# Performance work log

Measured on AMD Instinct MI355X. Metric: run time of the kernel, lower is better.

## Reference

```python
import jax, jax.numpy as jnp
import numpy as np

TEMPERATURE = 0.07
THRESHOLD = 0.7
NUM = 21          # config['data_loader']['args']['class_num']
EPS = 1e-12       # F.normalize eps
NEG_BIG = 1e30


def _nearest_down(x, H, W):
    # torch F.interpolate(mode='nearest'): in_idx = floor(out_idx * in/out)
    Hin, Win = x.shape[-2], x.shape[-1]
    ih = (jnp.arange(H) * Hin) // H
    iw = (jnp.arange(W) * Win) // W
    return x[..., ih[:, None], iw[None, :]]


def _l2n(x):
    return x / jnp.maximum(jnp.linalg.norm(x, axis=1, keepdims=True), EPS)


def setup_inputs() -> dict:
    key = jax.random.key(0)
    ks = jax.random.split(key, 6)
    B, C, H, W = 8, 256, 128, 128
    return {
        "labels": jax.random.randint(ks[0], (B, 512, 512), 0, NUM, dtype=jnp.int64)
        if jax.config.jax_enable_x64 else jax.random.randint(ks[0], (B, 512, 512), 0, NUM, dtype=jnp.int32),
        "features_old": jax.random.normal(ks[1], (B, C, H, W), dtype=jnp.float32),
        "features": jax.random.normal(ks[2], (B, C, H, W), dtype=jnp.float32),
        "outputs_old": jax.random.normal(ks[3], (B, 16, 512, 512), dtype=jnp.float32),
        "outputs": jax.random.normal(ks[4], (B, NUM, 512, 512), dtype=jnp.float32),
        "prototypes": jax.random.normal(ks[5], (NUM, C), dtype=jnp.float32),
        "num_class": 21,
        "num_old_class": 16,
        "num_new_class": 5,
        "epoch": 1,
        "train_step": 1,
        "len_epoch": 100,
    }


def reference(labels, features_old, features, outputs_old, outputs, prototypes,
              num_class, num_old_class, num_new_class, epoch, train_step, len_epoch):
    B, C, H, W = features.shape
    f32 = features.dtype

    # pseudo-label construction
    labels_down = _nearest_down(labels, H, W)                      # [B,H,W] int
    bgr_mask = (labels_down == 0).astype(labels_down.dtype)
    oo = jnp.where(outputs_old < THRESHOLD, 0.0, outputs_old)
    old_pred = jnp.argmax(oo, axis=1)                              # [B,512,512]
    old_down = _nearest_down(old_pred, H, W).astype(labels_down.dtype)
    pseudo = old_down * bgr_mask + labels_down                     # [B,H,W]
    lab = pseudo.reshape(-1)                                       # [N]
    mask = (lab >= 0) & (lab < NUM)

    # [N, C] normalized pixel features
    fa = _l2n(features.transpose(0, 2, 3, 1).reshape(-1, C))
    fo = _l2n(features_old.transpose(0, 2, 3, 1).reshape(-1, C))

    # per-class mean (segment reduce) replacing the python loop over unique labels
    seg = jnp.where(mask, lab, NUM)
    w = mask.astype(f32)
    counts = jax.ops.segment_sum(w, seg, num_segments=NUM + 1)[:NUM]          # [K]
    sum_a = jax.ops.segment_sum(fa * w[:, None], seg, num_segments=NUM + 1)[:NUM]
    sum_o = jax.ops.segment_sum(fo * w[:, None], seg, num_segments=NUM + 1)[:NUM]
    present = counts > 0
    denom = jnp.where(present, counts, 1.0)[:, None]
    anc = jnp.where(present[:, None], sum_a / denom, 0.0)          # [K,C] anchor prototypes
    con_prev = jnp.where(present[:, None], sum_o / denom, 0.0)     # [K,C] old prototypes
    contrast = jax.lax.stop_gradient(jnp.concatenate([anc, con_prev], axis=0))  # [2K,C]

    K = NUM
    eye = jnp.eye(K, dtype=f32)
    rowp = present.astype(f32)                                     # [K]
    colp = jnp.concatenate([rowp, rowp])                           # [2K]
    # labels are unique per row, so R = [I | I]; pos = [0 | I]; neg = 1 - R
    pos_mask = jnp.concatenate([jnp.zeros((K, K), f32), eye], axis=1) * rowp[:, None] * colp[None, :]
    neg_mask = (1.0 - jnp.concatenate([eye, eye], axis=1)) * rowp[:, None] * colp[None, :]

    adc = (anc @ contrast.T) / TEMPERATURE                         # [K,2K]
    # NOTE: faithful to source, negatives use UNshifted logits
    neg = jnp.sum(jnp.exp(adc) * neg_mask, axis=1, keepdims=True)  # [K,1]
    logits_max = jnp.max(jnp.where(colp[None, :] > 0, adc, -NEG_BIG), axis=1, keepdims=True)
    shifted = adc - jax.lax.stop_gradient(logits_max)
    pos_contrast = shifted * pos_mask - jnp.log(jnp.exp(shifted) + neg) * pos_mask

    num = pos_mask.sum(axis=1)
    valid = num > 0
    row_loss = -pos_contrast.sum(axis=1) / jnp.where(valid, num, 1.0)
    loss = jnp.sum(jnp.where(valid, row_loss, 0.0)) / jnp.maximum(jnp.sum(valid.astype(f32)), 1.0)
    return loss
```

## Files before the change

kernel.cpp:

```cpp
#include <hip/hip_runtime.h>
#include <math.h>

#define NPIX   131072
#define CCH    256
#define HW     16384
#define BSTR   4194304
#define NUMC   21
#define KC     5376
#define NREP   16

typedef __attribute__((ext_vector_type(8))) short bf16x8;
typedef __attribute__((ext_vector_type(4))) float f32x4;

static __device__ __forceinline__ uint f2bf(float x) {
    uint u = __builtin_bit_cast(uint, x);
    return (u + 0x7FFFu + ((u >> 16) & 1u)) >> 16;
}
static __device__ __forceinline__ uint ohv(int lbl, int cls, uint iv) {
    return (lbl == cls) ? iv : 0u;
}
static __device__ __forceinline__ float rsq_fast(float x) {
#if __has_builtin(__builtin_amdgcn_rsqf)
    return __builtin_amdgcn_rsqf(x);
#else
    return rsqrtf(x);
#endif
}
static __device__ __forceinline__ uint bfpack_trunc(float x, float y) {
    return __builtin_amdgcn_perm(__builtin_bit_cast(uint, y),
                                 __builtin_bit_cast(uint, x), 0x07060302u);
}

__global__ __launch_bounds__(256) void k_labels(const int* __restrict__ labels,
                                                const float* __restrict__ outputs_old,
                                                int* __restrict__ lab,
                                                float* __restrict__ gcnt)
{
    __shared__ float cnt[NUMC];
    if (threadIdx.x < NUMC) cnt[threadIdx.x] = 0.f;
    __syncthreads();

    int p = blockIdx.x * 256 + threadIdx.x;
    int b = p >> 14;
    int rem = p & 16383;
    int h = rem >> 7;
    int w = rem & 127;
    int ld = labels[b * 262144 + (h * 4) * 512 + (w * 4)];
    int out = ld;
    if (ld == 0) {
        const float* oo = outputs_old + (size_t)b * BSTR + (size_t)(h * 4) * 512 + (w * 4);
        float v0 = oo[0];
        float best = (v0 < 0.7f) ? 0.0f : v0;
        int bi = 0;
        #pragma unroll
        for (int c = 1; c < 16; ++c) {
            float v = oo[(size_t)c * 262144];
            v = (v < 0.7f) ? 0.0f : v;
            if (v > best) { best = v; bi = c; }
        }
        out = bi;
    }
    lab[p] = out;
    unsafeAtomicAdd(&cnt[out], 1.0f);
    __syncthreads();
    if (threadIdx.x < NUMC) unsafeAtomicAdd(&gcnt[threadIdx.x], cnt[threadIdx.x]);
}

__global__ __launch_bounds__(256, 2) void k_msum(const float* __restrict__ fa,
                                                 const float* __restrict__ fo,
                                                 const int* __restrict__ lab,
                                                 float* __restrict__ partA,
                                                 float* __restrict__ partO)
{
    __shared__ ushort tileB[CCH * 128];
    __shared__ float  ssqP[4][128];
    __shared__ float  invnS[128];
    __shared__ int    labS[256];

    const int t = threadIdx.x;
    const int w = t >> 6, l = t & 63;
    const int isO = blockIdx.x & 1;
    const float* __restrict__ src = isO ? fo : fa;
    float* part = isO ? partO : partA;

    const int pbase = (blockIdx.x >> 1) * 256;
    const int img   = pbase >> 14;
    const int hw0   = pbase & 16383;
    const float* g  = src + (size_t)img * BSTR + hw0;

    labS[t] = lab[pbase + t];

    f32x4 acc[2][4];
    #pragma unroll
    for (int m = 0; m < 2; ++m)
        #pragma unroll
        for (int n = 0; n < 4; ++n)
            acc[m][n] = (f32x4){0.f, 0.f, 0.f, 0.f};

#define LOADB(B, i0) do { \
    _Pragma("unroll") \
    for (int i_ = 0; i_ < 8; ++i_) \
        B[i_] = *(const float4*)(gc + (size_t)(w * 64 + 2 * ((i0) + i_) + (l >> 5)) * HW \
                                 + (l & 31) * 4); \
    } while (0)

#define PROCB(B, i0) do { \
    _Pragma("unroll") \
    for (int i_ = 0; i_ < 8; ++i_) { \
        float4 v_ = B[i_]; \
        s4.x += v_.x * v_.x;  s4.y += v_.y * v_.y; \
        s4.z += v_.z * v_.z;  s4.w += v_.w * v_.w; \
        int ch_ = w * 64 + 2 * ((i0) + i_) + (l >> 5); \
        uint lo_ = bfpack_trunc(v_.x, v_.y); \
        uint hi_ = bfpack_trunc(v_.z, v_.w); \
        *(uint2*)((char*)tileB + ch_ * 256 + ((((l & 31) * 8)) ^ ((ch_ & 7) << 4))) = \
            make_uint2(lo_, hi_); \
    } \
    } while (0)

#define KSTEP(c2, ks) do { \
    float4 ivA_ = *(const float4*)&invnS[(ks) * 32 + (l >> 4) * 8]; \
    float4 ivB_ = *(const float4*)&invnS[(ks) * 32 + (l >> 4) * 8 + 4]; \
    uint iv0 = f2bf(ivA_.x), iv1 = f2bf(ivA_.y), iv2 = f2bf(ivA_.z), iv3 = f2bf(ivA_.w); \
    uint iv4 = f2bf(ivB_.x), iv5 = f2bf(ivB_.y), iv6 = f2bf(ivB_.z), iv7 = f2bf(ivB_.w); \
    int4 la_ = *(const int4*)&labS[(c2) * 128 + (ks) * 32 + (l >> 4) * 8]; \
    int4 lb_ = *(const int4*)&labS[(c2) * 128 + (ks) * 32 + (l >> 4) * 8 + 4]; \
    const int cls0_ = l & 15, cls1_ = 16 + (l & 15); \
    uint4 u0_, u1_; \
    u0_.x = ohv(la_.x, cls0_, iv0) | (ohv(la_.y, cls0_, iv1) << 16); \
    u0_.y = ohv(la_.z, cls0_, iv2) | (ohv(la_.w, cls0_, iv3) << 16); \
    u0_.z = ohv(lb_.x, cls0_, iv4) | (ohv(lb_.y, cls0_, iv5) << 16); \
    u0_.w = ohv(lb_.z, cls0_, iv6) | (ohv(lb_.w, cls0_, iv7) << 16); \
    u1_.x = ohv(la_.x, cls1_, iv0) | (ohv(la_.y, cls1_, iv1) << 16); \
    u1_.y = ohv(la_.z, cls1_, iv2) | (ohv(la_.w, cls1_, iv3) << 16); \
    u1_.z = ohv(lb_.x, cls1_, iv4) | (ohv(lb_.y, cls1_, iv5) << 16); \
    u1_.w = ohv(lb_.z, cls1_, iv6) | (ohv(lb_.w, cls1_, iv7) << 16); \
    bf16x8 A0_ = __builtin_bit_cast(bf16x8, u0_); \
    bf16x8 A1_ = __builtin_bit_cast(bf16x8, u1_); \
    _Pragma("unroll") \
    for (int n_ = 0; n_ < 4; ++n_) { \
        const int chrow_ = (w * 4 + n_) * 16 + (l & 15); \
        const bf16x8 B_ = *(const bf16x8*)((const char*)tileB + chrow_ * 256 \
                            + (((ks) * 64 + (l >> 4) * 16) ^ ((chrow_ & 7) << 4))); \
        acc[0][n_] = __builtin_amdgcn_mfma_f32_16x16x32_bf16(A0_, B_, acc[0][n_], 0, 0, 0); \
        acc[1][n_] = __builtin_amdgcn_mfma_f32_16x16x32_bf16(A1_, B_, acc[1][n_], 0, 0, 0); \
    } \
    } while (0)

#define CHUNK(c2, LAST) do { \
    const float* gc = g + (c2) * 128; \
    float4 s4 = {0.f, 0.f, 0.f, 0.f}; \
    float4 bufA[8], bufB[8]; \
    LOADB(bufA, 0);  LOADB(bufB, 8); \
    PROCB(bufA, 0);  LOADB(bufA, 16); \
    PROCB(bufB, 8);  LOADB(bufB, 24); \
    PROCB(bufA, 16); PROCB(bufB, 24); \
    s4.x += __shfl_xor(s4.x, 32, 64);  s4.y += __shfl_xor(s4.y, 32, 64); \
    s4.z += __shfl_xor(s4.z, 32, 64);  s4.w += __shfl_xor(s4.w, 32, 64); \
    if (l < 32) *(float4*)&ssqP[w][l * 4] = s4; \
    __syncthreads(); \
    if (t < 128) { \
        float ss_ = ssqP[0][t] + ssqP[1][t] + ssqP[2][t] + ssqP[3][t]; \
        invnS[t] = rsq_fast(fmaxf(ss_, 1e-24f)); \
    } \
    __syncthreads(); \
    KSTEP(c2, 0); KSTEP(c2, 1); KSTEP(c2, 2); KSTEP(c2, 3); \
    if (!(LAST)) __syncthreads(); \
    } while (0)

    CHUNK(0, 0);
    CHUNK(1, 1);

#undef LOADB
#undef PROCB
#undef KSTEP
#undef CHUNK

    const int rep = (blockIdx.x >> 1) & (NREP - 1);
    #pragma unroll
    for (int m = 0; m < 2; ++m)
        #pragma unroll
        for (int n = 0; n < 4; ++n) {
            const int col = (w * 4 + n) * 16 + (l & 15);
            #pragma unroll
            for (int r = 0; r < 4; ++r) {
                const int row = m * 16 + (l >> 4) * 4 + r;
                if (row < NUMC)
                    unsafeAtomicAdd(&part[rep * KC + row * 256 + col], acc[m][n][r]);
            }
        }
}

__global__ __launch_bounds__(256) void k_final(const float* __restrict__ partA,
                                               const float* __restrict__ partO,
                                               const float* __restrict__ gcnt,
                                               float* __restrict__ out)
{
    __shared__ float anc[NUMC * 260];
    __shared__ float con[NUMC * 260];
    __shared__ float adc[NUMC * 44];
    __shared__ float cntS[NUMC];
    __shared__ float rowloss[NUMC];
    __shared__ float rowvalid[NUMC];

    if (threadIdx.x < NUMC) cntS[threadIdx.x] = gcnt[threadIdx.x];
    __syncthreads();
    for (int i = threadIdx.x; i < KC; i += 256) {
        float sA = 0.f, sO = 0.f;
        #pragma unroll
        for (int r = 0; r < NREP; ++r) { sA += partA[r * KC + i]; sO += partO[r * KC + i]; }
        int k = i >> 8, c = i & 255;
        float cn = cntS[k];
        bool pr = cn > 0.f;
        float d = pr ? cn : 1.f;
        anc[k * 260 + c] = pr ? sA / d : 0.f;
        con[k * 260 + c] = pr ? sO / d : 0.f;
    }
    __syncthreads();
    for (int pair = threadIdx.x; pair < NUMC * 2 * NUMC; pair += 256) {
        int k = pair / (2 * NUMC);
        int j = pair % (2 * NUMC);
        const float* ar = anc + k * 260;
        const float* br = (j < NUMC) ? (anc + j * 260) : (con + (j - NUMC) * 260);
        float s = 0.f;
        for (int c = 0; c < CCH; c += 4) {
            float4 a4 = *(const float4*)(ar + c);
            float4 b4 = *(const float4*)(br + c);
            s += a4.x * b4.x + a4.y * b4.y + a4.z * b4.z + a4.w * b4.w;
        }
        adc[k * 44 + j] = s / 0.07f;
    }
    __syncthreads();
    if (threadIdx.x < NUMC) {
        int k = threadIdx.x;
        bool pr = cntS[k] > 0.f;
        float neg = 0.f;
        float mx = -1e30f;
        for (int j = 0; j < 2 * NUMC; ++j) {
            int cj = (j < NUMC) ? j : (j - NUMC);
            bool cp = cntS[cj] > 0.f;
            float v = adc[k * 44 + j];
            if (cp) {
                if (v > mx) mx = v;
                if (j != k && j != NUMC + k) neg += expf(v);
            }
        }
        float sh = adc[k * 44 + NUMC + k] - mx;
        float rl = -(sh - logf(expf(sh) + neg));
        rowloss[k] = pr ? rl : 0.f;
        rowvalid[k] = pr ? 1.f : 0.f;
    }
    __syncthreads();
    if (threadIdx.x == 0) {
        float s = 0.f, v = 0.f;
        for (int kk = 0; kk < NUMC; ++kk) { s += rowloss[kk]; v += rowvalid[kk]; }
        out[0] = s / fmaxf(v, 1.f);
    }
}

extern "C" void kernel_launch(void* const* d_in, const int* in_sizes, int n_in,
                              void* d_out, int out_size, void* d_ws, size_t ws_size,
                              hipStream_t stream) {
    const int*   labels      = (const int*)  d_in[0];
    const float* feats_old   = (const float*)d_in[1];
    const float* feats       = (const float*)d_in[2];
    const float* outputs_old = (const float*)d_in[3];

    float* ws    = (float*)d_ws;
    int*   lab   = (int*)ws;
    float* partA = ws + 131072;
    float* partO = partA + NREP * KC;
    float* gcnt  = partO + NREP * KC;

    hipMemsetAsync(partA, 0, (size_t)(2 * NREP * KC + NUMC) * sizeof(float), stream);

    k_labels<<<NPIX / 256, 256, 0, stream>>>(labels, outputs_old, lab, gcnt);
    k_msum  <<<1024, 256, 0, stream>>>(feats, feats_old, lab, partA, partO);
    k_final <<<1, 256, 0, stream>>>(partA, partO, gcnt, (float*)d_out);
}
```

Before: 97.43 us.

## Shrink msum pixel tiles, drop memset, and replace global count atomics with partials

k_msum now processes 64 pixels per block instead of 256, launching 4096 blocks with a smaller LDS tile and a launch bound allowing 4 blocks per CU, to raise occupancy and memory-level parallelism. The hipMemsetAsync is removed: k_labels zeroes the partial-sum buffers itself (512 blocks x 336 floats covers 2*16*5376), and writes per-block class counts, which k_final reduces. This removes a separate launch and global atomics on the counts. In exchange it adds 4x more global atomic flushes of the MFMA partials into the 16 replicas, raising contention.

```diff
diff --git a/kernel.cpp b/kernel.cpp
--- a/kernel.cpp
+++ b/kernel.cpp
@@ -8,6 +8,7 @@
 #define NUMC   21
 #define KC     5376
 #define NREP   16
+#define NLB    512
 
 typedef __attribute__((ext_vector_type(8))) short bf16x8;
 typedef __attribute__((ext_vector_type(4))) float f32x4;
@@ -34,11 +35,17 @@
 __global__ __launch_bounds__(256) void k_labels(const int* __restrict__ labels,
                                                 const float* __restrict__ outputs_old,
                                                 int* __restrict__ lab,
-                                                float* __restrict__ gcnt)
+                                                float* __restrict__ cntPart,
+                                                float* __restrict__ partzero)
 {
     __shared__ float cnt[NUMC];
     if (threadIdx.x < NUMC) cnt[threadIdx.x] = 0.f;
     __syncthreads();
+
+    {
+        float* pz = partzero + blockIdx.x * 336;
+        for (int i = threadIdx.x; i < 336; i += 256) pz[i] = 0.f;
+    }
 
     int p = blockIdx.x * 256 + threadIdx.x;
     int b = p >> 14;
@@ -63,19 +70,21 @@
     lab[p] = out;
     unsafeAtomicAdd(&cnt[out], 1.0f);
     __syncthreads();
-    if (threadIdx.x < NUMC) unsafeAtomicAdd(&gcnt[threadIdx.x], cnt[threadIdx.x]);
-}
-
-__global__ __launch_bounds__(256, 2) void k_msum(const float* __restrict__ fa,
+    if (threadIdx.x < 32)
+        cntPart[blockIdx.x * 32 + threadIdx.x] =
+            (threadIdx.x < NUMC) ? cnt[threadIdx.x] : 0.f;
+}
+
+__global__ __launch_bounds__(256, 4) void k_msum(const float* __restrict__ fa,
                                                  const float* __restrict__ fo,
                                                  const int* __restrict__ lab,
                                                  float* __restrict__ partA,
                                                  float* __restrict__ partO)
 {
-    __shared__ ushort tileB[CCH * 128];
-    __shared__ float  ssqP[4][128];
-    __shared__ float  invnS[128];
-    __shared__ int    labS[256];
+    __shared__ ushort tileB[CCH * 64];
+    __shared__ float  ssqP[4][64];
+    __shared__ float  invnS[64];
+    __shared__ int    labS[64];
 
     const int t = threadIdx.x;
     const int w = t >> 6, l = t & 63;
@@ -83,12 +92,12 @@
     const float* __restrict__ src = isO ? fo : fa;
     float* part = isO ? partO : partA;
 
-    const int pbase = (blockIdx.x >> 1) * 256;
+    const int pbase = (blockIdx.x >> 1) * 64;
     const int img   = pbase >> 14;
     const int hw0   = pbase & 16383;
     const float* g  = src + (size_t)img * BSTR + hw0;
 
-    labS[t] = lab[pbase + t];
+    if (t < 64) labS[t] = lab[pbase + t];
 
     f32x4 acc[2][4];
     #pragma unroll
@@ -100,8 +109,8 @@
 #define LOADB(B, i0) do { \
     _Pragma("unroll") \
     for (int i_ = 0; i_ < 8; ++i_) \
-        B[i_] = *(const float4*)(gc + (size_t)(w * 64 + 2 * ((i0) + i_) + (l >> 5)) * HW \
-                                 + (l & 31) * 4); \
+        B[i_] = *(const float4*)(g + (size_t)(w * 64 + 4 * ((i0) + i_) + (l >> 4)) * HW \
+                                 + (l & 15) * 4); \
     } while (0)
 
 #define PROCB(B, i0) do { \
@@ -110,21 +119,21 @@
         float4 v_ = B[i_]; \
         s4.x += v_.x * v_.x;  s4.y += v_.y * v_.y; \
         s4.z += v_.z * v_.z;  s4.w += v_.w * v_.w; \
-        int ch_ = w * 64 + 2 * ((i0) + i_) + (l >> 5); \
+        int ch_ = w * 64 + 4 * ((i0) + i_) + (l >> 4); \
         uint lo_ = bfpack_trunc(v_.x, v_.y); \
         uint hi_ = bfpack_trunc(v_.z, v_.w); \
-        *(uint2*)((char*)tileB + ch_ * 256 + ((((l & 31) * 8)) ^ ((ch_ & 7) << 4))) = \
+        *(uint2*)((char*)tileB + ch_ * 128 + (((l & 15) * 8) ^ ((ch_ & 7) << 4))) = \
             make_uint2(lo_, hi_); \
     } \
     } while (0)
 
-#define KSTEP(c2, ks) do { \
+#define KSTEP(ks) do { \
     float4 ivA_ = *(const float4*)&invnS[(ks) * 32 + (l >> 4) * 8]; \
     float4 ivB_ = *(const float4*)&invnS[(ks) * 32 + (l >> 4) * 8 + 4]; \
     uint iv0 = f2bf(ivA_.x), iv1 = f2bf(ivA_.y), iv2 = f2bf(ivA_.z), iv3 = f2bf(ivA_.w); \
     uint iv4 = f2bf(ivB_.x), iv5 = f2bf(ivB_.y), iv6 = f2bf(ivB_.z), iv7 = f2bf(ivB_.w); \
-    int4 la_ = *(const int4*)&labS[(c2) * 128 + (ks) * 32 + (l >> 4) * 8]; \
-    int4 lb_ = *(const int4*)&labS[(c2) * 128 + (ks) * 32 + (l >> 4) * 8 + 4]; \
+    int4 la_ = *(const int4*)&labS[(ks) * 32 + (l >> 4) * 8]; \
+    int4 lb_ = *(const int4*)&labS[(ks) * 32 + (l >> 4) * 8 + 4]; \
     const int cls0_ = l & 15, cls1_ = 16 + (l & 15); \
     uint4 u0_, u1_; \
     u0_.x = ohv(la_.x, cls0_, iv0) | (ohv(la_.y, cls0_, iv1) << 16); \
@@ -140,41 +149,35 @@
     _Pragma("unroll") \
     for (int n_ = 0; n_ < 4; ++n_) { \
         const int chrow_ = (w * 4 + n_) * 16 + (l & 15); \
-        const bf16x8 B_ = *(const bf16x8*)((const char*)tileB + chrow_ * 256 \
+        const bf16x8 B_ = *(const bf16x8*)((const char*)tileB + chrow_ * 128 \
                             + (((ks) * 64 + (l >> 4) * 16) ^ ((chrow_ & 7) << 4))); \
         acc[0][n_] = __builtin_amdgcn_mfma_f32_16x16x32_bf16(A0_, B_, acc[0][n_], 0, 0, 0); \
         acc[1][n_] = __builtin_amdgcn_mfma_f32_16x16x32_bf16(A1_, B_, acc[1][n_], 0, 0, 0); \
     } \
     } while (0)
 
-#define CHUNK(c2, LAST) do { \
-    const float* gc = g + (c2) * 128; \
-    float4 s4 = {0.f, 0.f, 0.f, 0.f}; \
-    float4 bufA[8], bufB[8]; \
-    LOADB(bufA, 0);  LOADB(bufB, 8); \
-    PROCB(bufA, 0);  LOADB(bufA, 16); \
-    PROCB(bufB, 8);  LOADB(bufB, 24); \
-    PROCB(bufA, 16); PROCB(bufB, 24); \
-    s4.x += __shfl_xor(s4.x, 32, 64);  s4.y += __shfl_xor(s4.y, 32, 64); \
-    s4.z += __shfl_xor(s4.z, 32, 64);  s4.w += __shfl_xor(s4.w, 32, 64); \
-    if (l < 32) *(float4*)&ssqP[w][l * 4] = s4; \
-    __syncthreads(); \
-    if (t < 128) { \
-        float ss_ = ssqP[0][t] + ssqP[1][t] + ssqP[2][t] + ssqP[3][t]; \
-        invnS[t] = rsq_fast(fmaxf(ss_, 1e-24f)); \
-    } \
-    __syncthreads(); \
-    KSTEP(c2, 0); KSTEP(c2, 1); KSTEP(c2, 2); KSTEP(c2, 3); \
-    if (!(LAST)) __syncthreads(); \
-    } while (0)
-
-    CHUNK(0, 0);
-    CHUNK(1, 1);
+    float4 bufA[8], bufB[8];
+    float4 s4 = {0.f, 0.f, 0.f, 0.f};
+    LOADB(bufA, 0);
+    LOADB(bufB, 8);
+    PROCB(bufA, 0);
+    PROCB(bufB, 8);
+    s4.x += __shfl_xor(s4.x, 16, 64);  s4.y += __shfl_xor(s4.y, 16, 64);
+    s4.z += __shfl_xor(s4.z, 16, 64);  s4.w += __shfl_xor(s4.w, 16, 64);
+    s4.x += __shfl_xor(s4.x, 32, 64);  s4.y += __shfl_xor(s4.y, 32, 64);
+    s4.z += __shfl_xor(s4.z, 32, 64);  s4.w += __shfl_xor(s4.w, 32, 64);
+    if (l < 16) *(float4*)&ssqP[w][l * 4] = s4;
+    __syncthreads();
+    if (t < 64)
+        invnS[t] = rsq_fast(fmaxf(ssqP[0][t] + ssqP[1][t] + ssqP[2][t] + ssqP[3][t],
+                                  1e-24f));
+    __syncthreads();
+    KSTEP(0);
+    KSTEP(1);
 
 #undef LOADB
 #undef PROCB
 #undef KSTEP
-#undef CHUNK
 
     const int rep = (blockIdx.x >> 1) & (NREP - 1);
     #pragma unroll
@@ -193,18 +196,22 @@
 
 __global__ __launch_bounds__(256) void k_final(const float* __restrict__ partA,
                                                const float* __restrict__ partO,
-                                               const float* __restrict__ gcnt,
+                                               const float* __restrict__ cntPart,
                                                float* __restrict__ out)
 {
     __shared__ float anc[NUMC * 260];
     __shared__ float con[NUMC * 260];
     __shared__ float adc[NUMC * 44];
-    __shared__ float cntS[NUMC];
+    __shared__ float cntS[32];
     __shared__ float rowloss[NUMC];
     __shared__ float rowvalid[NUMC];
 
-    if (threadIdx.x < NUMC) cntS[threadIdx.x] = gcnt[threadIdx.x];
-    __syncthreads();
+    if (threadIdx.x < 32) cntS[threadIdx.x] = 0.f;
+    __syncthreads();
+    for (int i = threadIdx.x; i < NLB * 32; i += 256)
+        unsafeAtomicAdd(&cntS[i & 31], cntPart[i]);
+    __syncthreads();
+
     for (int i = threadIdx.x; i < KC; i += 256) {
         float sA = 0.f, sO = 0.f;
         #pragma unroll
@@ -266,15 +273,14 @@
     const float* feats       = (const float*)d_in[2];
     const float* outputs_old = (const float*)d_in[3];
 
-    float* ws    = (float*)d_ws;
-    int*   lab   = (int*)ws;
-    float* partA = ws + 131072;
-    float* partO = partA + NREP * KC;
-    float* gcnt  = partO + NREP * KC;
-
-    hipMemsetAsync(partA, 0, (size_t)(2 * NREP * KC + NUMC) * sizeof(float), stream);
-
-    k_labels<<<NPIX / 256, 256, 0, stream>>>(labels, outputs_old, lab, gcnt);
-    k_msum  <<<1024, 256, 0, stream>>>(feats, feats_old, lab, partA, partO);
-    k_final <<<1, 256, 0, stream>>>(partA, partO, gcnt, (float*)d_out);
-}
+    float* ws      = (float*)d_ws;
+    int*   lab     = (int*)ws;
+    float* partA   = ws + 131072;
+    float* partO   = partA + NREP * KC;
+    float* cntPart = partO + NREP * KC;
+
+
+    k_labels<<<NLB, 256, 0, stream>>>(labels, outputs_old, lab, cntPart, partA);
+    k_msum  <<<4096, 256, 0, stream>>>(feats, feats_old, lab, partA, partO);
+    k_final <<<1, 256, 0, stream>>>(partA, partO, cntPart, (float*)d_out);
+}
```

Result: slower. 137.5 us (+41.1%).

## Fuse label computation into feature-sum kernel and parallelize partial reduction

Applied to the files above, without the earlier changes.

Removes the separate label kernel: each block of the fused kernel now computes its own pseudo-labels (both the A and O blocks recompute them) while the first feature loads are in flight. The second channel chunk's loads are also issued before the first chunk's MFMA step, to overlap memory with compute. Class counts are written as per-block partials, and a new 43-block reduction kernel sums the replicas before the single-block final kernel. This saves a launch and a global round trip for labels, at the cost of duplicated outputs_old reads, higher register pressure from the extra buffers, and an added small kernel.

```diff
diff --git a/kernel.cpp b/kernel.cpp
--- a/kernel.cpp
+++ b/kernel.cpp
@@ -31,51 +31,19 @@
                                  __builtin_bit_cast(uint, x), 0x07060302u);
 }
 
-__global__ __launch_bounds__(256) void k_labels(const int* __restrict__ labels,
-                                                const float* __restrict__ outputs_old,
-                                                int* __restrict__ lab,
-                                                float* __restrict__ gcnt)
-{
-    __shared__ float cnt[NUMC];
-    if (threadIdx.x < NUMC) cnt[threadIdx.x] = 0.f;
-    __syncthreads();
-
-    int p = blockIdx.x * 256 + threadIdx.x;
-    int b = p >> 14;
-    int rem = p & 16383;
-    int h = rem >> 7;
-    int w = rem & 127;
-    int ld = labels[b * 262144 + (h * 4) * 512 + (w * 4)];
-    int out = ld;
-    if (ld == 0) {
-        const float* oo = outputs_old + (size_t)b * BSTR + (size_t)(h * 4) * 512 + (w * 4);
-        float v0 = oo[0];
-        float best = (v0 < 0.7f) ? 0.0f : v0;
-        int bi = 0;
-        #pragma unroll
-        for (int c = 1; c < 16; ++c) {
-            float v = oo[(size_t)c * 262144];
-            v = (v < 0.7f) ? 0.0f : v;
-            if (v > best) { best = v; bi = c; }
-        }
-        out = bi;
-    }
-    lab[p] = out;
-    unsafeAtomicAdd(&cnt[out], 1.0f);
-    __syncthreads();
-    if (threadIdx.x < NUMC) unsafeAtomicAdd(&gcnt[threadIdx.x], cnt[threadIdx.x]);
-}
-
-__global__ __launch_bounds__(256, 2) void k_msum(const float* __restrict__ fa,
-                                                 const float* __restrict__ fo,
-                                                 const int* __restrict__ lab,
-                                                 float* __restrict__ partA,
-                                                 float* __restrict__ partO)
+__global__ __launch_bounds__(256, 2) void k_fused(const int* __restrict__ labels,
+                                                  const float* __restrict__ outputs_old,
+                                                  const float* __restrict__ fa,
+                                                  const float* __restrict__ fo,
+                                                  float* __restrict__ partA,
+                                                  float* __restrict__ partO,
+                                                  float* __restrict__ cntPart)
 {
     __shared__ ushort tileB[CCH * 128];
     __shared__ float  ssqP[4][128];
     __shared__ float  invnS[128];
     __shared__ int    labS[256];
+    __shared__ float  cnt[32];
 
     const int t = threadIdx.x;
     const int w = t >> 6, l = t & 63;
@@ -87,8 +55,6 @@
     const int img   = pbase >> 14;
     const int hw0   = pbase & 16383;
     const float* g  = src + (size_t)img * BSTR + hw0;
-
-    labS[t] = lab[pbase + t];
 
     f32x4 acc[2][4];
     #pragma unroll
@@ -97,11 +63,11 @@
         for (int n = 0; n < 4; ++n)
             acc[m][n] = (f32x4){0.f, 0.f, 0.f, 0.f};
 
-#define LOADB(B, i0) do { \
+#define LOADB(B, i0, c2) do { \
     _Pragma("unroll") \
     for (int i_ = 0; i_ < 8; ++i_) \
-        B[i_] = *(const float4*)(gc + (size_t)(w * 64 + 2 * ((i0) + i_) + (l >> 5)) * HW \
-                                 + (l & 31) * 4); \
+        B[i_] = *(const float4*)(g + (size_t)(w * 64 + 2 * ((i0) + i_) + (l >> 5)) * HW \
+                                 + (c2) * 128 + (l & 31) * 4); \
     } while (0)
 
 #define PROCB(B, i0) do { \
@@ -147,34 +113,76 @@
     } \
     } while (0)
 
-#define CHUNK(c2, LAST) do { \
-    const float* gc = g + (c2) * 128; \
-    float4 s4 = {0.f, 0.f, 0.f, 0.f}; \
-    float4 bufA[8], bufB[8]; \
-    LOADB(bufA, 0);  LOADB(bufB, 8); \
-    PROCB(bufA, 0);  LOADB(bufA, 16); \
-    PROCB(bufB, 8);  LOADB(bufB, 24); \
-    PROCB(bufA, 16); PROCB(bufB, 24); \
-    s4.x += __shfl_xor(s4.x, 32, 64);  s4.y += __shfl_xor(s4.y, 32, 64); \
-    s4.z += __shfl_xor(s4.z, 32, 64);  s4.w += __shfl_xor(s4.w, 32, 64); \
-    if (l < 32) *(float4*)&ssqP[w][l * 4] = s4; \
-    __syncthreads(); \
-    if (t < 128) { \
-        float ss_ = ssqP[0][t] + ssqP[1][t] + ssqP[2][t] + ssqP[3][t]; \
-        invnS[t] = rsq_fast(fmaxf(ss_, 1e-24f)); \
-    } \
-    __syncthreads(); \
-    KSTEP(c2, 0); KSTEP(c2, 1); KSTEP(c2, 2); KSTEP(c2, 3); \
-    if (!(LAST)) __syncthreads(); \
-    } while (0)
-
-    CHUNK(0, 0);
-    CHUNK(1, 1);
+    float4 bufA[8], bufB[8];
+    float4 s4;
+
+    LOADB(bufA, 0, 0);
+    LOADB(bufB, 8, 0);
+
+    if (t < 32) cnt[t] = 0.f;
+    __syncthreads();
+    {
+        const int p   = pbase + t;
+        const int rem = p & 16383;
+        const int hh  = rem >> 7;
+        const int ww2 = rem & 127;
+        int ld = labels[img * 262144 + hh * 4 * 512 + ww2 * 4];
+        int out = ld;
+        if (ld == 0) {
+            const float* oo = outputs_old + (size_t)img * BSTR
+                              + (size_t)(hh * 4) * 512 + ww2 * 4;
+            float v0 = oo[0];
+            float best = (v0 < 0.7f) ? 0.0f : v0;
+            int bi = 0;
+            #pragma unroll
+            for (int c = 1; c < 16; ++c) {
+                float v = oo[(size_t)c * 262144];
+                v = (v < 0.7f) ? 0.0f : v;
+                if (v > best) { best = v; bi = c; }
+            }
+            out = bi;
+        }
+        labS[t] = out;
+        if (!isO) unsafeAtomicAdd(&cnt[out], 1.0f);
+    }
+    __syncthreads();
+    if (!isO && t < 32)
+        cntPart[(blockIdx.x >> 1) * 32 + t] = (t < NUMC) ? cnt[t] : 0.f;
+
+    s4 = (float4){0.f, 0.f, 0.f, 0.f};
+    PROCB(bufA, 0);  LOADB(bufA, 16, 0);
+    PROCB(bufB, 8);  LOADB(bufB, 24, 0);
+    PROCB(bufA, 16); PROCB(bufB, 24);
+    s4.x += __shfl_xor(s4.x, 32, 64);  s4.y += __shfl_xor(s4.y, 32, 64);
+    s4.z += __shfl_xor(s4.z, 32, 64);  s4.w += __shfl_xor(s4.w, 32, 64);
+    if (l < 32) *(float4*)&ssqP[w][l * 4] = s4;
+    LOADB(bufA, 0, 1);
+    LOADB(bufB, 8, 1);
+    __syncthreads();
+    if (t < 128)
+        invnS[t] = rsq_fast(fmaxf(ssqP[0][t] + ssqP[1][t] + ssqP[2][t] + ssqP[3][t],
+                                  1e-24f));
+    __syncthreads();
+    KSTEP(0, 0); KSTEP(0, 1); KSTEP(0, 2); KSTEP(0, 3);
+    __syncthreads();
+
+    s4 = (float4){0.f, 0.f, 0.f, 0.f};
+    PROCB(bufA, 0);  LOADB(bufA, 16, 1);
+    PROCB(bufB, 8);  LOADB(bufB, 24, 1);
+    PROCB(bufA, 16); PROCB(bufB, 24);
+    s4.x += __shfl_xor(s4.x, 32, 64);  s4.y += __shfl_xor(s4.y, 32, 64);
+    s4.z += __shfl_xor(s4.z, 32, 64);  s4.w += __shfl_xor(s4.w, 32, 64);
+    if (l < 32) *(float4*)&ssqP[w][l * 4] = s4;
+    __syncthreads();
+    if (t < 128)
+        invnS[t] = rsq_fast(fmaxf(ssqP[0][t] + ssqP[1][t] + ssqP[2][t] + ssqP[3][t],
+                                  1e-24f));
+    __syncthreads();
+    KSTEP(1, 0); KSTEP(1, 1); KSTEP(1, 2); KSTEP(1, 3);
 
 #undef LOADB
 #undef PROCB
 #undef KSTEP
-#undef CHUNK
 
     const int rep = (blockIdx.x >> 1) & (NREP - 1);
     #pragma unroll
@@ -191,10 +199,35 @@
         }
 }
 
-__global__ __launch_bounds__(256) void k_final(const float* __restrict__ partA,
-                                               const float* __restrict__ partO,
-                                               const float* __restrict__ gcnt,
-                                               float* __restrict__ out)
+__global__ __launch_bounds__(256) void k_red(const float* __restrict__ partA,
+                                             const float* __restrict__ partO,
+                                             const float* __restrict__ cntPart,
+                                             float* __restrict__ gsum,
+                                             float* __restrict__ gcnt)
+{
+    const int b = blockIdx.x, t = threadIdx.x;
+    if (b < 42) {
+        const float* part = (b < 21) ? partA : partO;
+        const int cls = (b < 21) ? b : b - 21;
+        float s = 0.f;
+        #pragma unroll
+        for (int r = 0; r < NREP; ++r) s += part[r * KC + cls * 256 + t];
+        gsum[b * 256 + t] = s;
+    } else {
+        __shared__ float cs[32];
+        if (t < 32) cs[t] = 0.f;
+        __syncthreads();
+        float s = 0.f;
+        for (int i = t; i < 512 * 32; i += 256) s += cntPart[i];
+        unsafeAtomicAdd(&cs[t & 31], s);
+        __syncthreads();
+        if (t < NUMC) gcnt[t] = cs[t];
+    }
+}
+
+__global__ __launch_bounds__(256) void k_final2(const float* __restrict__ gsum,
+                                                const float* __restrict__ gcnt,
+                                                float* __restrict__ out)
 {
     __shared__ float anc[NUMC * 260];
     __shared__ float con[NUMC * 260];
@@ -206,15 +239,12 @@
     if (threadIdx.x < NUMC) cntS[threadIdx.x] = gcnt[threadIdx.x];
     __syncthreads();
     for (int i = threadIdx.x; i < KC; i += 256) {
-        float sA = 0.f, sO = 0.f;
-        #pragma unroll
-        for (int r = 0; r < NREP; ++r) { sA += partA[r * KC + i]; sO += partO[r * KC + i]; }
         int k = i >> 8, c = i & 255;
         float cn = cntS[k];
         bool pr = cn > 0.f;
         float d = pr ? cn : 1.f;
-        anc[k * 260 + c] = pr ? sA / d : 0.f;
-        con[k * 260 + c] = pr ? sO / d : 0.f;
+        anc[k * 260 + c] = pr ? gsum[k * 256 + c] / d : 0.f;
+        con[k * 260 + c] = pr ? gsum[(NUMC + k) * 256 + c] / d : 0.f;
     }
     __syncthreads();
     for (int pair = threadIdx.x; pair < NUMC * 2 * NUMC; pair += 256) {
@@ -266,15 +296,17 @@
     const float* feats       = (const float*)d_in[2];
     const float* outputs_old = (const float*)d_in[3];
 
-    float* ws    = (float*)d_ws;
-    int*   lab   = (int*)ws;
-    float* partA = ws + 131072;
-    float* partO = partA + NREP * KC;
-    float* gcnt  = partO + NREP * KC;
-
-    hipMemsetAsync(partA, 0, (size_t)(2 * NREP * KC + NUMC) * sizeof(float), stream);
-
-    k_labels<<<NPIX / 256, 256, 0, stream>>>(labels, outputs_old, lab, gcnt);
-    k_msum  <<<1024, 256, 0, stream>>>(feats, feats_old, lab, partA, partO);
-    k_final <<<1, 256, 0, stream>>>(partA, partO, gcnt, (float*)d_out);
-}
+    float* ws      = (float*)d_ws;
+    float* partA   = ws;
+    float* partO   = partA + NREP * KC;
+    float* cntPart = partO + NREP * KC;
+    float* gsum    = cntPart + 512 * 32;
+    float* gcnt    = gsum + 42 * 256;
+
+    hipMemsetAsync(partA, 0, (size_t)(2 * NREP * KC) * sizeof(float), stream);
+
+    k_fused <<<1024, 256, 0, stream>>>(labels, outputs_old, feats, feats_old,
+                                       partA, partO, cntPart);
+    k_red   <<<43, 256, 0, stream>>>(partA, partO, cntPart, gsum, gcnt);
+    k_final2<<<1, 256, 0, stream>>>(gsum, gcnt, (float*)d_out);
+}
```

New measurement: 107.8 us. +10.6%, slower.
